# Kernel tuning notes

Measured on AMD Instinct MI355X. Metric: run time of the kernel, lower is better.

Reference implementation:

```python
import jax, jax.numpy as jnp
import numpy as np

B, S, E = 4, 2048, 1024


def setup_inputs() -> dict:
    key = jax.random.key(0)
    ks = jax.random.split(key, 7)
    s = 1.0 / np.sqrt(E)  # torch Linear default init scale (uniform bound)
    inp = {
        "input": jax.random.normal(ks[0], (B, S, E), dtype=jnp.float32),
        "masked": 1,
        "W_q": jax.random.uniform(ks[1], (E, E), jnp.float32, -s, s),
        "b_q": jax.random.uniform(ks[2], (E,), jnp.float32, -s, s),
        "W_k": jax.random.uniform(ks[3], (E, E), jnp.float32, -s, s),
        "b_k": jax.random.uniform(ks[4], (E,), jnp.float32, -s, s),
        "W_v": jax.random.uniform(ks[5], (E, E), jnp.float32, -s, s),
        "b_v": jax.random.uniform(ks[6], (E,), jnp.float32, -s, s),
    }
    return inp


def reference(input, masked, W_q, b_q, W_k, b_k, W_v, b_v):
    # torch.nn.Linear: y = x @ W.T + b
    q = jnp.einsum("bse,fe->bsf", input, W_q) + b_q
    k = jnp.einsum("bse,fe->bsf", input, W_k) + b_k
    v = jnp.einsum("bse,fe->bsf", input, W_v) + b_v
    d = q.shape[-1]
    scores = jnp.einsum("bqd,bkd->bqk", q, k) / jnp.sqrt(jnp.float32(d))
    if masked:
        Sq = scores.shape[1]
        causal = jnp.tril(jnp.ones((Sq, Sq), dtype=bool))  # [S,S], broadcast over batch
        scores = jnp.where(causal, scores, -jnp.inf)
    attn = jax.nn.softmax(scores, axis=-1)
    return jnp.einsum("bqk,bkd->bqd", attn, v)
```

## Files before the change

kernel.cpp:

```cpp
#include <hip/hip_runtime.h>

typedef _Float16 f16;
typedef f16 f16x8 __attribute__((ext_vector_type(8)));
typedef f16 f16x4v __attribute__((ext_vector_type(4)));
typedef float f32x4 __attribute__((ext_vector_type(4)));

__device__ __forceinline__ void async_ld16(const void* g, void* l) {
    __builtin_amdgcn_global_load_lds(
        (const __attribute__((address_space(1))) unsigned int*)g,
        (__attribute__((address_space(3))) unsigned int*)l, 16, 0, 0);
}


#define STG(b, op, kh, P, P1, tOff) do {                                        \
    char* d_ = (char*)smem + (b) * 65536 + (op) * 32768 + (kh) * 16384 + stgBase; \
    async_ld16((P)  + (tOff) * 64 + (kh) * 32, d_);                             \
    async_ld16((P1) + (tOff) * 64 + (kh) * 32, d_ + 8192);                      \
} while (0)
#define RD_A(b, kk) do {                                                        \
    const char* s_ = (const char*)smem + (b) * 65536 + (kk) * 16384 + aOff;     \
    _Pragma("unroll") for (int m_ = 0; m_ < 8; ++m_)                            \
        af[m_] = *(const f16x8*)(s_ + m_ * 1024);                               \
} while (0)
#define RD_B2(b, kk, n0_) do {                                                  \
    const char* s_ = (const char*)smem + (b) * 65536 + 32768 + (kk) * 16384 + bOff; \
    bf[(n0_)]     = *(const f16x8*)(s_ + ((n0_)) * 1024);                       \
    bf[(n0_) + 1] = *(const f16x8*)(s_ + ((n0_) + 1) * 1024);                   \
} while (0)
#define FENCE_MM(n0_) do {                                                      \
    __builtin_amdgcn_s_barrier();                                               \
    asm volatile("s_waitcnt lgkmcnt(0)" ::: "memory");                          \
    __builtin_amdgcn_sched_barrier(0);                                          \
    __builtin_amdgcn_s_setprio(1);                                              \
    _Pragma("unroll") for (int m_ = 0; m_ < 8; ++m_) {                          \
        acc[m_][(n0_)]     = __builtin_amdgcn_mfma_f32_16x16x32_f16(af[m_], bf[(n0_)],     acc[m_][(n0_)],     0, 0, 0); \
        acc[m_][(n0_) + 1] = __builtin_amdgcn_mfma_f32_16x16x32_f16(af[m_], bf[(n0_) + 1], acc[m_][(n0_) + 1], 0, 0, 0); \
    }                                                                           \
    __builtin_amdgcn_s_setprio(0);                                              \
} while (0)
#define VMC(n) asm volatile("s_waitcnt vmcnt(" #n ")" ::: "memory")
#define BAR __builtin_amdgcn_s_barrier()

#define GEMM256_MAIN_LOOP do {                                                  \
    STG(0, 0, 0, pA, pA1, 0); STG(0, 1, 0, pB, pB1, 0);                         \
    STG(0, 0, 1, pA, pA1, 0); STG(0, 1, 1, pB, pB1, 0);                         \
    STG(1, 0, 0, pA, pA1, 1); STG(1, 1, 0, pB, pB1, 1);                         \
    VMC(4);                                                                     \
    BAR;                                                                        \
    _Pragma("unroll 1")                                                         \
    for (int i_ = 0; i_ < 7; ++i_) {                                            \
        RD_A(0, 0); RD_B2(0, 0, 0); STG(1, 0, 1, pA, pA1, 1);           \
        FENCE_MM(0); BAR;                                                       \
        RD_B2(0, 0, 2);             STG(1, 1, 1, pB, pB1, 1);           \
        FENCE_MM(2); BAR;                                                       \
        RD_A(0, 1); RD_B2(0, 1, 0); STG(0, 0, 0, pA, pA1, 2);           \
        FENCE_MM(0); BAR;                                                       \
        RD_B2(0, 1, 2);             STG(0, 1, 0, pB, pB1, 2);           \
        FENCE_MM(2); VMC(4); BAR;                                               \
        RD_A(1, 0); RD_B2(1, 0, 0); STG(0, 0, 1, pA, pA1, 2);           \
        FENCE_MM(0); BAR;                                                       \
        RD_B2(1, 0, 2);             STG(0, 1, 1, pB, pB1, 2);           \
        FENCE_MM(2); BAR;                                                       \
        RD_A(1, 1); RD_B2(1, 1, 0); STG(1, 0, 0, pA, pA1, 3);           \
        FENCE_MM(0); BAR;                                                       \
        RD_B2(1, 1, 2);             STG(1, 1, 0, pB, pB1, 3);           \
        FENCE_MM(2); VMC(4); BAR;                                               \
        pA += 128; pA1 += 128; pB += 128; pB1 += 128;                           \
    }                                                                           \
    RD_A(0, 0); RD_B2(0, 0, 0); STG(1, 0, 1, pA, pA1, 1);                       \
    FENCE_MM(0); BAR;                                                           \
    RD_B2(0, 0, 2);             STG(1, 1, 1, pB, pB1, 1);                       \
    FENCE_MM(2); BAR;                                                           \
    RD_A(0, 1); RD_B2(0, 1, 0);                                                 \
    FENCE_MM(0); BAR;                                                           \
    RD_B2(0, 1, 2);                                                             \
    FENCE_MM(2); VMC(0); BAR;                                                   \
    RD_A(1, 0); RD_B2(1, 0, 0);                                                 \
    FENCE_MM(0); BAR;                                                           \
    RD_B2(1, 0, 2);                                                             \
    FENCE_MM(2); BAR;                                                           \
    RD_A(1, 1); RD_B2(1, 1, 0);                                                 \
    FENCE_MM(0); BAR;                                                           \
    RD_B2(1, 1, 2);                                                             \
    FENCE_MM(2); BAR;        \
} while (0)

#define GEMM256_SETUP                                                           \
    __shared__ __align__(16) f16 smem[65536];                      \
    const int tid = threadIdx.x;                                                \
    const int wave = tid >> 6, lane = tid & 63;                                 \
    const int wrow = wave >> 2, wcol = wave & 3;                                \
    const int quad = lane >> 4, l16 = lane & 15;                                \
    const int rowLane = tid >> 2;                                               \
    const int cOff = ((tid & 3) ^ ((tid >> 3) & 3)) * 8;                        \
    const int stgBase = wave * 1024;                                            \
    const int swz  = (quad ^ ((l16 >> 1) & 3)) * 16;                            \
    const int aOff = (wrow * 128 + l16) * 64 + swz;                             \
    const int bOff = (wcol * 64 + l16) * 64 + swz;                              \
    f32x4 acc[8][4];                                                            \
    _Pragma("unroll") for (int m_i = 0; m_i < 8; ++m_i)                         \
        _Pragma("unroll") for (int n_i = 0; n_i < 4; ++n_i)                     \
            acc[m_i][n_i] = (f32x4){0.f, 0.f, 0.f, 0.f};                        \
    f16x8 af[8], bf[4];

__global__ __launch_bounds__(512, 2) void qkv256(
    const f16* __restrict__ A, const f16* __restrict__ Bt,
    const float* __restrict__ b_q, const float* __restrict__ b_k,
    const float* __restrict__ b_v,
    f16* __restrict__ Q16, f16* __restrict__ K16, f16* __restrict__ Vt16)
{
    int bid = blockIdx.x;
    bid = (bid & 7) * 48 + (bid >> 3);
    const int by = bid / 12, bx = bid - by * 12;
    const int mBase = by * 256, nBase = bx * 256;

    GEMM256_SETUP

    const f16* pA  = A  + (long)(mBase + rowLane) * 1024 + cOff;
    const f16* pA1 = pA + 128 * 1024;
    const f16* pB  = Bt + (long)(nBase + rowLane) * 1024 + cOff;
    const f16* pB1 = pB + 128 * 1024;

    GEMM256_MAIN_LOOP;

    const int seg = nBase >> 10;
    const float* bs = (seg == 0) ? b_q : (seg == 1) ? b_k : b_v;
    const int lcb = (nBase & 1023) + wcol * 64;
    float bvv[4];
#pragma unroll
    for (int n = 0; n < 4; ++n) bvv[n] = bs[lcb + n * 16 + l16];

    if (seg < 2) {
        f16* dst = (seg == 0) ? Q16 : K16;
#pragma unroll
        for (int m = 0; m < 8; ++m)
#pragma unroll
            for (int n = 0; n < 4; ++n)
#pragma unroll
                for (int r = 0; r < 4; ++r) {
                    const int row = mBase + wrow * 128 + m * 16 + quad * 4 + r;
                    dst[(long)row * 1024 + lcb + n * 16 + l16] =
                        (f16)(acc[m][n][r] + bvv[n]);
                }
    } else {
        const int b = mBase >> 11, s0 = mBase & 2047;
        const int e0 = (nBase & 1023) + wcol * 64;
        f16* epiW = smem + wave * (64 * 80);
#pragma unroll
        for (int sb = 0; sb < 2; ++sb) {
#pragma unroll
            for (int m4 = 0; m4 < 4; ++m4)
#pragma unroll
                for (int n = 0; n < 4; ++n) {
                    f16x4v pk;
#pragma unroll
                    for (int r = 0; r < 4; ++r)
                        pk[r] = (f16)(acc[sb * 4 + m4][n][r] + bvv[n]);
                    *(f16x4v*)&epiW[(n * 16 + l16) * 80 + m4 * 16 + quad * 4] = pk;
                }
            asm volatile("s_waitcnt lgkmcnt(0)" ::: "memory");
#pragma unroll
            for (int it = 0; it < 8; ++it) {
                const int e = it * 8 + (lane >> 3);
                const f16x8 v = *(const f16x8*)&epiW[e * 80 + (lane & 7) * 8];
                *(f16x8*)(Vt16 + ((long)b * 1024 + e0 + e) * 2048 + s0 +
                          wrow * 128 + sb * 64 + (lane & 7) * 8) = v;
            }
        }
    }
}

__global__ __launch_bounds__(512, 2) void scores256(
    const f16* __restrict__ Q, const f16* __restrict__ K,
    f16* __restrict__ P, float* __restrict__ rowsum,
    const int* __restrict__ maskedp)
{
    const int masked = *maskedp;
    const int bx = blockIdx.x, by = blockIdx.y, bz = blockIdx.z;
    if (masked && bx > by) return;
    const int mBase = by * 256, nBase = bx * 256;

    GEMM256_SETUP

    const f16* Ab  = Q + (long)bz * (2048L * 1024);
    const f16* Btb = K + (long)bz * (2048L * 1024);
    const f16* pA  = Ab  + (long)(mBase + rowLane) * 1024 + cOff;
    const f16* pA1 = pA + 128 * 1024;
    const f16* pB  = Btb + (long)(nBase + rowLane) * 1024 + cOff;
    const f16* pB1 = pB + 128 * 1024;

    GEMM256_MAIN_LOOP;

    f16* Crow = P + (long)bz * (2048L * 2048);
    float* rsb = rowsum + bz * 2048;
#pragma unroll
    for (int m = 0; m < 8; ++m) {
        float rs[4] = {0.f, 0.f, 0.f, 0.f};
#pragma unroll
        for (int n = 0; n < 4; ++n)
#pragma unroll
            for (int r = 0; r < 4; ++r) {
                const int row = mBase + wrow * 128 + m * 16 + quad * 4 + r;
                const int col = nBase + wcol * 64 + n * 16 + l16;
                float e = __expf(acc[m][n][r] * 0.03125f);
                if (masked && col > row) e = 0.f;
                const f16 hv = (f16)e;
                Crow[(long)row * 2048 + col] = hv;
                rs[r] += (float)hv;
            }
#pragma unroll
        for (int r = 0; r < 4; ++r) {
            float s = rs[r];
            s += __shfl_xor(s, 1);
            s += __shfl_xor(s, 2);
            s += __shfl_xor(s, 4);
            s += __shfl_xor(s, 8);
            if (l16 == 0) {
                const int row = mBase + wrow * 128 + m * 16 + quad * 4 + r;
                atomicAdd(&rsb[row], s);
            }
        }
    }
}

#undef STG
#undef RD_A
#undef RD_B2
#undef FENCE_MM
#undef GEMM256_MAIN_LOOP
#undef GEMM256_SETUP

#define PSTG_A(b, kh, tOff) do {                                                \
    char* d_ = (char*)smem + (b) * 32768 + (kh) * 8192 + stgBase;               \
    async_ld16(pA  + (tOff) * 64 + (kh) * 32, d_);                              \
    async_ld16(pA1 + (tOff) * 64 + (kh) * 32, d_ + 4096);                       \
} while (0)
#define PSTG_B(b, kh, tOff) do {                                                \
    char* d_ = (char*)smem + (b) * 32768 + 16384 + (kh) * 8192 + stgBase;       \
    async_ld16(pB  + (tOff) * 64 + (kh) * 32, d_);                              \
    async_ld16(pB1 + (tOff) * 64 + (kh) * 32, d_ + 4096);                       \
} while (0)
#define PRD(b, kk) do {                                                         \
    const char* sa_ = (const char*)smem + (b) * 32768 + (kk) * 8192 + aOff;     \
    _Pragma("unroll") for (int m_ = 0; m_ < 4; ++m_)                            \
        af[m_] = *(const f16x8*)(sa_ + m_ * 1024);                              \
    const char* sb_ = (const char*)smem + (b) * 32768 + 16384 + (kk) * 8192 + bOff; \
    _Pragma("unroll") for (int n_ = 0; n_ < 4; ++n_)                            \
        bf[n_] = *(const f16x8*)(sb_ + n_ * 1024);                              \
} while (0)
#define PFENCE do {                                                             \
    __builtin_amdgcn_s_barrier();                                               \
    asm volatile("s_waitcnt lgkmcnt(0)" ::: "memory");                          \
    __builtin_amdgcn_sched_barrier(0);                                          \
    __builtin_amdgcn_s_setprio(1);                                              \
    _Pragma("unroll") for (int m_ = 0; m_ < 4; ++m_)                            \
        _Pragma("unroll") for (int n_ = 0; n_ < 4; ++n_)                        \
            acc[m_][n_] = __builtin_amdgcn_mfma_f32_16x16x32_f16(af[m_], bf[n_], acc[m_][n_], 0, 0, 0); \
    __builtin_amdgcn_s_setprio(0);                                              \
} while (0)

__global__ __launch_bounds__(256, 2) void pv128(
    const f16* __restrict__ P, const f16* __restrict__ Vt,
    const float* __restrict__ rowsum, float* __restrict__ out,
    const int* __restrict__ maskedp)
{
    const int masked = *maskedp;
    const int bx = blockIdx.x, bz = blockIdx.z;
    const int by = gridDim.y - 1 - blockIdx.y;
    const int mBase = by * 128, nBase = bx * 128;
    const int nIter = masked ? ((by >> 1) + 1) * 2 : 16;

    __shared__ __align__(16) f16 smem[32768];
    const int tid = threadIdx.x;
    const int wave = tid >> 6, lane = tid & 63;
    const int wrow = wave >> 1, wcol = wave & 1;
    const int quad = lane >> 4, l16 = lane & 15;
    const int rowLane = tid >> 2;
    const int cOff = ((tid & 3) ^ ((tid >> 3) & 3)) * 8;
    const int stgBase = wave * 1024;
    const int swz  = (quad ^ ((l16 >> 1) & 3)) * 16;
    const int aOff = (wrow * 64 + l16) * 64 + swz;
    const int bOff = (wcol * 64 + l16) * 64 + swz;

    const f16* Pb = P  + (long)bz * (2048L * 2048);
    const f16* Vb = Vt + (long)bz * (1024L * 2048);
    const f16* pA  = Pb + (long)(mBase + rowLane) * 2048 + cOff;
    const f16* pA1 = pA + 64 * 2048;
    const f16* pB  = Vb + (long)(nBase + rowLane) * 2048 + cOff;
    const f16* pB1 = pB + 64 * 2048;

    f32x4 acc[4][4];
#pragma unroll
    for (int m = 0; m < 4; ++m)
#pragma unroll
        for (int n = 0; n < 4; ++n) acc[m][n] = (f32x4){0.f, 0.f, 0.f, 0.f};
    f16x8 af[4], bf[4];

    PSTG_A(0, 0, 0); PSTG_B(0, 0, 0);
    PSTG_A(0, 1, 0); PSTG_B(0, 1, 0);
    PSTG_A(1, 0, 1); PSTG_B(1, 0, 1);
    VMC(4);
    BAR;

#pragma unroll 1
    for (int i = 0; i < nIter - 1; ++i) {
        PRD(0, 0); PSTG_A(1, 1, 1); PSTG_B(1, 1, 1);
        PFENCE; VMC(8); BAR;
        PRD(0, 1); PSTG_A(0, 0, 2); PSTG_B(0, 0, 2);
        PFENCE; VMC(8); BAR;
        PRD(1, 0); PSTG_A(0, 1, 2); PSTG_B(0, 1, 2);
        PFENCE; VMC(8); BAR;
        PRD(1, 1); PSTG_A(1, 0, 3); PSTG_B(1, 0, 3);
        PFENCE; VMC(8); BAR;
        pA += 128; pA1 += 128; pB += 128; pB1 += 128;
    }
    PRD(0, 0); PSTG_A(1, 1, 1); PSTG_B(1, 1, 1);
    PFENCE; VMC(8); BAR;
    PRD(0, 1);
    PFENCE; VMC(4); BAR;
    PRD(1, 0);
    PFENCE; VMC(0); BAR;
    PRD(1, 1);
    PFENCE;

    const float* rsb = rowsum + bz * 2048;
    float* ob = out + (long)bz * (2048L * 1024);
#pragma unroll
    for (int m = 0; m < 4; ++m)
#pragma unroll
        for (int r = 0; r < 4; ++r) {
            const int row = mBase + wrow * 64 + m * 16 + quad * 4 + r;
            const float inv = 1.f / rsb[row];
#pragma unroll
            for (int n = 0; n < 4; ++n) {
                const int col = nBase + wcol * 64 + n * 16 + l16;
                ob[(long)row * 1024 + col] = acc[m][n][r] * inv;
            }
        }
}

#undef PSTG_A
#undef PSTG_B
#undef PRD
#undef PFENCE
#undef VMC
#undef BAR

__global__ void cvt_inp(const float* __restrict__ in, f16* __restrict__ out, int n4)
{
    const int i = blockIdx.x * blockDim.x + threadIdx.x;
    if (i >= n4) return;
    const float4 v = ((const float4*)in)[i];
    f16x4v o;
    o[0] = (f16)v.x; o[1] = (f16)v.y; o[2] = (f16)v.z; o[3] = (f16)v.w;
    ((f16x4v*)out)[i] = o;
}

__global__ void cvt_w3(const float* __restrict__ W0, const float* __restrict__ W1,
                       const float* __restrict__ W2, f16* __restrict__ out)
{
    const int bxx = blockIdx.x;
    const int which = bxx >> 10;
    const float* src = (which == 0) ? W0 : (which == 1) ? W1 : W2;
    const int i = (bxx & 1023) * 256 + threadIdx.x;
    const float4 v = ((const float4*)src)[i];
    f16x4v o;
    o[0] = (f16)v.x; o[1] = (f16)v.y; o[2] = (f16)v.z; o[3] = (f16)v.w;
    ((f16x4v*)(out + (long)which * 1024 * 1024))[i] = o;
}

extern "C" void kernel_launch(void* const* d_in, const int* in_sizes, int n_in,
                              void* d_out, int out_size, void* d_ws, size_t ws_size,
                              hipStream_t stream)
{
    const float* inp = (const float*)d_in[0];
    const int* masked = (const int*)d_in[1];
    const float* Wq = (const float*)d_in[2];
    const float* bq = (const float*)d_in[3];
    const float* Wk = (const float*)d_in[4];
    const float* bk = (const float*)d_in[5];
    const float* Wv = (const float*)d_in[6];
    const float* bv = (const float*)d_in[7];
    float* out = (float*)d_out;

    const int Bb = 4, S = 2048, E = 1024;
    const long nTok = (long)Bb * S;

    char* ws = (char*)d_ws;
    f16* inp16 = (f16*)ws;   ws += nTok * E * 2;
    f16* W3    = (f16*)ws;   ws += (long)3 * E * E * 2;
    f16* Q16   = (f16*)ws;   ws += nTok * E * 2;
    f16* K16   = (f16*)ws;   ws += nTok * E * 2;
    f16* Vt16  = (f16*)ws;   ws += nTok * E * 2;
    f16* P16   = (f16*)ws;   ws += (long)Bb * S * S * 2;
    float* rsum = (float*)ws; ws += nTok * 4;

    dim3 blk(256);

    hipMemsetAsync(rsum, 0, nTok * 4, stream);
    cvt_inp<<<(int)(nTok * E / 4 / 256), blk, 0, stream>>>(inp, inp16, (int)(nTok * E / 4));
    cvt_w3<<<3 * 1024, blk, 0, stream>>>(Wq, Wk, Wv, W3);

    qkv256<<<dim3(32 * 12), dim3(512), 0, stream>>>(
        inp16, W3, bq, bk, bv, Q16, K16, Vt16);

    scores256<<<dim3(8, 8, 4), dim3(512), 0, stream>>>(
        Q16, K16, P16, rsum, masked);

    pv128<<<dim3(8, 16, 4), dim3(256), 0, stream>>>(
        P16, Vt16, rsum, out, masked);
}
```

Before: 241.5 us.

## Replace 256x256 QKV GEMM tile with 128x256 tile kernel

The fused QKV projection GEMM moves from a 256x256 block tile to a 128x256 tile, doubling the grid from 384 to 768 blocks. This gives better wave coverage of the CUs, where 384 blocks would leave a partial second wave. The new kernel has a smaller LDS footprint, a 4x4 MFMA accumulator per wave, and a simpler four-phase pipeline with adjusted vmcnt waits. The smaller tile has lower arithmetic intensity, so operand traffic per FLOP goes up. The shared macros are inlined into the scores kernel.

```diff
diff --git a/kernel.cpp b/kernel.cpp
--- a/kernel.cpp
+++ b/kernel.cpp
@@ -11,6 +11,8 @@
         (__attribute__((address_space(3))) unsigned int*)l, 16, 0, 0);
 }
 
+#define VMC(n) asm volatile("s_waitcnt vmcnt(" #n ")" ::: "memory")
+#define BAR __builtin_amdgcn_s_barrier()
 
 #define STG(b, op, kh, P, P1, tOff) do {                                        \
     char* d_ = (char*)smem + (b) * 65536 + (op) * 32768 + (kh) * 16384 + stgBase; \
@@ -38,137 +40,6 @@
     }                                                                           \
     __builtin_amdgcn_s_setprio(0);                                              \
 } while (0)
-#define VMC(n) asm volatile("s_waitcnt vmcnt(" #n ")" ::: "memory")
-#define BAR __builtin_amdgcn_s_barrier()
-
-#define GEMM256_MAIN_LOOP do {                                                  \
-    STG(0, 0, 0, pA, pA1, 0); STG(0, 1, 0, pB, pB1, 0);                         \
-    STG(0, 0, 1, pA, pA1, 0); STG(0, 1, 1, pB, pB1, 0);                         \
-    STG(1, 0, 0, pA, pA1, 1); STG(1, 1, 0, pB, pB1, 1);                         \
-    VMC(4);                                                                     \
-    BAR;                                                                        \
-    _Pragma("unroll 1")                                                         \
-    for (int i_ = 0; i_ < 7; ++i_) {                                            \
-        RD_A(0, 0); RD_B2(0, 0, 0); STG(1, 0, 1, pA, pA1, 1);           \
-        FENCE_MM(0); BAR;                                                       \
-        RD_B2(0, 0, 2);             STG(1, 1, 1, pB, pB1, 1);           \
-        FENCE_MM(2); BAR;                                                       \
-        RD_A(0, 1); RD_B2(0, 1, 0); STG(0, 0, 0, pA, pA1, 2);           \
-        FENCE_MM(0); BAR;                                                       \
-        RD_B2(0, 1, 2);             STG(0, 1, 0, pB, pB1, 2);           \
-        FENCE_MM(2); VMC(4); BAR;                                               \
-        RD_A(1, 0); RD_B2(1, 0, 0); STG(0, 0, 1, pA, pA1, 2);           \
-        FENCE_MM(0); BAR;                                                       \
-        RD_B2(1, 0, 2);             STG(0, 1, 1, pB, pB1, 2);           \
-        FENCE_MM(2); BAR;                                                       \
-        RD_A(1, 1); RD_B2(1, 1, 0); STG(1, 0, 0, pA, pA1, 3);           \
-        FENCE_MM(0); BAR;                                                       \
-        RD_B2(1, 1, 2);             STG(1, 1, 0, pB, pB1, 3);           \
-        FENCE_MM(2); VMC(4); BAR;                                               \
-        pA += 128; pA1 += 128; pB += 128; pB1 += 128;                           \
-    }                                                                           \
-    RD_A(0, 0); RD_B2(0, 0, 0); STG(1, 0, 1, pA, pA1, 1);                       \
-    FENCE_MM(0); BAR;                                                           \
-    RD_B2(0, 0, 2);             STG(1, 1, 1, pB, pB1, 1);                       \
-    FENCE_MM(2); BAR;                                                           \
-    RD_A(0, 1); RD_B2(0, 1, 0);                                                 \
-    FENCE_MM(0); BAR;                                                           \
-    RD_B2(0, 1, 2);                                                             \
-    FENCE_MM(2); VMC(0); BAR;                                                   \
-    RD_A(1, 0); RD_B2(1, 0, 0);                                                 \
-    FENCE_MM(0); BAR;                                                           \
-    RD_B2(1, 0, 2);                                                             \
-    FENCE_MM(2); BAR;                                                           \
-    RD_A(1, 1); RD_B2(1, 1, 0);                                                 \
-    FENCE_MM(0); BAR;                                                           \
-    RD_B2(1, 1, 2);                                                             \
-    FENCE_MM(2); BAR;        \
-} while (0)
-
-#define GEMM256_SETUP                                                           \
-    __shared__ __align__(16) f16 smem[65536];                      \
-    const int tid = threadIdx.x;                                                \
-    const int wave = tid >> 6, lane = tid & 63;                                 \
-    const int wrow = wave >> 2, wcol = wave & 3;                                \
-    const int quad = lane >> 4, l16 = lane & 15;                                \
-    const int rowLane = tid >> 2;                                               \
-    const int cOff = ((tid & 3) ^ ((tid >> 3) & 3)) * 8;                        \
-    const int stgBase = wave * 1024;                                            \
-    const int swz  = (quad ^ ((l16 >> 1) & 3)) * 16;                            \
-    const int aOff = (wrow * 128 + l16) * 64 + swz;                             \
-    const int bOff = (wcol * 64 + l16) * 64 + swz;                              \
-    f32x4 acc[8][4];                                                            \
-    _Pragma("unroll") for (int m_i = 0; m_i < 8; ++m_i)                         \
-        _Pragma("unroll") for (int n_i = 0; n_i < 4; ++n_i)                     \
-            acc[m_i][n_i] = (f32x4){0.f, 0.f, 0.f, 0.f};                        \
-    f16x8 af[8], bf[4];
-
-__global__ __launch_bounds__(512, 2) void qkv256(
-    const f16* __restrict__ A, const f16* __restrict__ Bt,
-    const float* __restrict__ b_q, const float* __restrict__ b_k,
-    const float* __restrict__ b_v,
-    f16* __restrict__ Q16, f16* __restrict__ K16, f16* __restrict__ Vt16)
-{
-    int bid = blockIdx.x;
-    bid = (bid & 7) * 48 + (bid >> 3);
-    const int by = bid / 12, bx = bid - by * 12;
-    const int mBase = by * 256, nBase = bx * 256;
-
-    GEMM256_SETUP
-
-    const f16* pA  = A  + (long)(mBase + rowLane) * 1024 + cOff;
-    const f16* pA1 = pA + 128 * 1024;
-    const f16* pB  = Bt + (long)(nBase + rowLane) * 1024 + cOff;
-    const f16* pB1 = pB + 128 * 1024;
-
-    GEMM256_MAIN_LOOP;
-
-    const int seg = nBase >> 10;
-    const float* bs = (seg == 0) ? b_q : (seg == 1) ? b_k : b_v;
-    const int lcb = (nBase & 1023) + wcol * 64;
-    float bvv[4];
-#pragma unroll
-    for (int n = 0; n < 4; ++n) bvv[n] = bs[lcb + n * 16 + l16];
-
-    if (seg < 2) {
-        f16* dst = (seg == 0) ? Q16 : K16;
-#pragma unroll
-        for (int m = 0; m < 8; ++m)
-#pragma unroll
-            for (int n = 0; n < 4; ++n)
-#pragma unroll
-                for (int r = 0; r < 4; ++r) {
-                    const int row = mBase + wrow * 128 + m * 16 + quad * 4 + r;
-                    dst[(long)row * 1024 + lcb + n * 16 + l16] =
-                        (f16)(acc[m][n][r] + bvv[n]);
-                }
-    } else {
-        const int b = mBase >> 11, s0 = mBase & 2047;
-        const int e0 = (nBase & 1023) + wcol * 64;
-        f16* epiW = smem + wave * (64 * 80);
-#pragma unroll
-        for (int sb = 0; sb < 2; ++sb) {
-#pragma unroll
-            for (int m4 = 0; m4 < 4; ++m4)
-#pragma unroll
-                for (int n = 0; n < 4; ++n) {
-                    f16x4v pk;
-#pragma unroll
-                    for (int r = 0; r < 4; ++r)
-                        pk[r] = (f16)(acc[sb * 4 + m4][n][r] + bvv[n]);
-                    *(f16x4v*)&epiW[(n * 16 + l16) * 80 + m4 * 16 + quad * 4] = pk;
-                }
-            asm volatile("s_waitcnt lgkmcnt(0)" ::: "memory");
-#pragma unroll
-            for (int it = 0; it < 8; ++it) {
-                const int e = it * 8 + (lane >> 3);
-                const f16x8 v = *(const f16x8*)&epiW[e * 80 + (lane & 7) * 8];
-                *(f16x8*)(Vt16 + ((long)b * 1024 + e0 + e) * 2048 + s0 +
-                          wrow * 128 + sb * 64 + (lane & 7) * 8) = v;
-            }
-        }
-    }
-}
 
 __global__ __launch_bounds__(512, 2) void scores256(
     const f16* __restrict__ Q, const f16* __restrict__ K,
@@ -180,7 +51,23 @@
     if (masked && bx > by) return;
     const int mBase = by * 256, nBase = bx * 256;
 
-    GEMM256_SETUP
+    __shared__ __align__(16) f16 smem[65536];
+    const int tid = threadIdx.x;
+    const int wave = tid >> 6, lane = tid & 63;
+    const int wrow = wave >> 2, wcol = wave & 3;
+    const int quad = lane >> 4, l16 = lane & 15;
+    const int rowLane = tid >> 2;
+    const int cOff = ((tid & 3) ^ ((tid >> 3) & 3)) * 8;
+    const int stgBase = wave * 1024;
+    const int swz  = (quad ^ ((l16 >> 1) & 3)) * 16;
+    const int aOff = (wrow * 128 + l16) * 64 + swz;
+    const int bOff = (wcol * 64 + l16) * 64 + swz;
+    f32x4 acc[8][4];
+#pragma unroll
+    for (int m = 0; m < 8; ++m)
+#pragma unroll
+        for (int n = 0; n < 4; ++n) acc[m][n] = (f32x4){0.f, 0.f, 0.f, 0.f};
+    f16x8 af[8], bf[4];
 
     const f16* Ab  = Q + (long)bz * (2048L * 1024);
     const f16* Btb = K + (long)bz * (2048L * 1024);
@@ -189,7 +76,48 @@
     const f16* pB  = Btb + (long)(nBase + rowLane) * 1024 + cOff;
     const f16* pB1 = pB + 128 * 1024;
 
-    GEMM256_MAIN_LOOP;
+    STG(0, 0, 0, pA, pA1, 0); STG(0, 1, 0, pB, pB1, 0);
+    STG(0, 0, 1, pA, pA1, 0); STG(0, 1, 1, pB, pB1, 0);
+    STG(1, 0, 0, pA, pA1, 1); STG(1, 1, 0, pB, pB1, 1);
+    VMC(4);
+    BAR;
+
+#pragma unroll 1
+    for (int i = 0; i < 7; ++i) {
+        RD_A(0, 0); RD_B2(0, 0, 0); STG(1, 0, 1, pA, pA1, 1);
+        FENCE_MM(0); BAR;
+        RD_B2(0, 0, 2);             STG(1, 1, 1, pB, pB1, 1);
+        FENCE_MM(2); BAR;
+        RD_A(0, 1); RD_B2(0, 1, 0); STG(0, 0, 0, pA, pA1, 2);
+        FENCE_MM(0); BAR;
+        RD_B2(0, 1, 2);             STG(0, 1, 0, pB, pB1, 2);
+        FENCE_MM(2); VMC(4); BAR;
+        RD_A(1, 0); RD_B2(1, 0, 0); STG(0, 0, 1, pA, pA1, 2);
+        FENCE_MM(0); BAR;
+        RD_B2(1, 0, 2);             STG(0, 1, 1, pB, pB1, 2);
+        FENCE_MM(2); BAR;
+        RD_A(1, 1); RD_B2(1, 1, 0); STG(1, 0, 0, pA, pA1, 3);
+        FENCE_MM(0); BAR;
+        RD_B2(1, 1, 2);             STG(1, 1, 0, pB, pB1, 3);
+        FENCE_MM(2); VMC(4); BAR;
+        pA += 128; pA1 += 128; pB += 128; pB1 += 128;
+    }
+    RD_A(0, 0); RD_B2(0, 0, 0); STG(1, 0, 1, pA, pA1, 1);
+    FENCE_MM(0); BAR;
+    RD_B2(0, 0, 2);             STG(1, 1, 1, pB, pB1, 1);
+    FENCE_MM(2); BAR;
+    RD_A(0, 1); RD_B2(0, 1, 0);
+    FENCE_MM(0); BAR;
+    RD_B2(0, 1, 2);
+    FENCE_MM(2); VMC(0); BAR;
+    RD_A(1, 0); RD_B2(1, 0, 0);
+    FENCE_MM(0); BAR;
+    RD_B2(1, 0, 2);
+    FENCE_MM(2); BAR;
+    RD_A(1, 1); RD_B2(1, 1, 0);
+    FENCE_MM(0); BAR;
+    RD_B2(1, 1, 2);
+    FENCE_MM(2);
 
     f16* Crow = P + (long)bz * (2048L * 2048);
     float* rsb = rowsum + bz * 2048;
@@ -227,8 +155,146 @@
 #undef RD_A
 #undef RD_B2
 #undef FENCE_MM
-#undef GEMM256_MAIN_LOOP
-#undef GEMM256_SETUP
+
+#define QSTG_A(b, kh, tOff) do {                                                \
+    char* d_ = (char*)smem + (b) * 49152 + (kh) * 8192 + stgBase;               \
+    async_ld16(pA + (tOff) * 64 + (kh) * 32, d_);                               \
+} while (0)
+#define QSTG_B(b, kh, tOff) do {                                                \
+    char* d_ = (char*)smem + (b) * 49152 + 16384 + (kh) * 16384 + stgBase;      \
+    async_ld16(pB  + (tOff) * 64 + (kh) * 32, d_);                              \
+    async_ld16(pB1 + (tOff) * 64 + (kh) * 32, d_ + 8192);                       \
+} while (0)
+#define QRD(b, kk) do {                                                         \
+    const char* sa_ = (const char*)smem + (b) * 49152 + (kk) * 8192 + aOff;     \
+    _Pragma("unroll") for (int m_ = 0; m_ < 4; ++m_)                            \
+        af[m_] = *(const f16x8*)(sa_ + m_ * 1024);                              \
+    const char* sb_ = (const char*)smem + (b) * 49152 + 16384 + (kk) * 16384 + bOff; \
+    _Pragma("unroll") for (int n_ = 0; n_ < 4; ++n_)                            \
+        bf[n_] = *(const f16x8*)(sb_ + n_ * 1024);                              \
+} while (0)
+#define QFENCE do {                                                             \
+    __builtin_amdgcn_s_barrier();                                               \
+    asm volatile("s_waitcnt lgkmcnt(0)" ::: "memory");                          \
+    __builtin_amdgcn_sched_barrier(0);                                          \
+    __builtin_amdgcn_s_setprio(1);                                              \
+    _Pragma("unroll") for (int m_ = 0; m_ < 4; ++m_)                            \
+        _Pragma("unroll") for (int n_ = 0; n_ < 4; ++n_)                        \
+            acc[m_][n_] = __builtin_amdgcn_mfma_f32_16x16x32_f16(af[m_], bf[n_], acc[m_][n_], 0, 0, 0); \
+    __builtin_amdgcn_s_setprio(0);                                              \
+} while (0)
+
+__global__ __launch_bounds__(512, 2) void qkv128(
+    const f16* __restrict__ A, const f16* __restrict__ Bt,
+    const float* __restrict__ b_q, const float* __restrict__ b_k,
+    const float* __restrict__ b_v,
+    f16* __restrict__ Q16, f16* __restrict__ K16, f16* __restrict__ Vt16)
+{
+    int bid = blockIdx.x;
+    bid = (bid & 7) * 96 + (bid >> 3);
+    const int by = bid / 12, bx = bid - by * 12;
+    const int mBase = by * 128, nBase = bx * 256;
+
+    __shared__ __align__(16) f16 smem[49152];
+    const int tid = threadIdx.x;
+    const int wave = tid >> 6, lane = tid & 63;
+    const int wrow = wave >> 2, wcol = wave & 3;
+    const int quad = lane >> 4, l16 = lane & 15;
+    const int rowLane = tid >> 2;
+    const int cOff = ((tid & 3) ^ ((tid >> 3) & 3)) * 8;
+    const int stgBase = wave * 1024;
+    const int swz  = (quad ^ ((l16 >> 1) & 3)) * 16;
+    const int aOff = (wrow * 64 + l16) * 64 + swz;
+    const int bOff = (wcol * 64 + l16) * 64 + swz;
+
+    const f16* pA  = A  + (long)(mBase + rowLane) * 1024 + cOff;
+    const f16* pB  = Bt + (long)(nBase + rowLane) * 1024 + cOff;
+    const f16* pB1 = pB + 128 * 1024;
+
+    f32x4 acc[4][4];
+#pragma unroll
+    for (int m = 0; m < 4; ++m)
+#pragma unroll
+        for (int n = 0; n < 4; ++n) acc[m][n] = (f32x4){0.f, 0.f, 0.f, 0.f};
+    f16x8 af[4], bf[4];
+
+    QSTG_A(0, 0, 0); QSTG_B(0, 0, 0);
+    QSTG_A(0, 1, 0); QSTG_B(0, 1, 0);
+    QSTG_A(1, 0, 1); QSTG_B(1, 0, 1);
+    VMC(3);
+    BAR;
+
+#pragma unroll 1
+    for (int i = 0; i < 7; ++i) {
+        QRD(0, 0); QSTG_A(1, 1, 1); QSTG_B(1, 1, 1);
+        QFENCE; VMC(6); BAR;
+        QRD(0, 1); QSTG_A(0, 0, 2); QSTG_B(0, 0, 2);
+        QFENCE; VMC(6); BAR;
+        QRD(1, 0); QSTG_A(0, 1, 2); QSTG_B(0, 1, 2);
+        QFENCE; VMC(6); BAR;
+        QRD(1, 1); QSTG_A(1, 0, 3); QSTG_B(1, 0, 3);
+        QFENCE; VMC(6); BAR;
+        pA += 128; pB += 128; pB1 += 128;
+    }
+    QRD(0, 0); QSTG_A(1, 1, 1); QSTG_B(1, 1, 1);
+    QFENCE; VMC(6); BAR;
+    QRD(0, 1);
+    QFENCE; VMC(3); BAR;
+    QRD(1, 0);
+    QFENCE; VMC(0); BAR;
+    QRD(1, 1);
+    QFENCE;
+    BAR;
+
+    const int seg = nBase >> 10;
+    const float* bs = (seg == 0) ? b_q : (seg == 1) ? b_k : b_v;
+    const int lcb = (nBase & 1023) + wcol * 64;
+    float bvv[4];
+#pragma unroll
+    for (int n = 0; n < 4; ++n) bvv[n] = bs[lcb + n * 16 + l16];
+
+    if (seg < 2) {
+        f16* dst = (seg == 0) ? Q16 : K16;
+#pragma unroll
+        for (int m = 0; m < 4; ++m)
+#pragma unroll
+            for (int n = 0; n < 4; ++n)
+#pragma unroll
+                for (int r = 0; r < 4; ++r) {
+                    const int row = mBase + wrow * 64 + m * 16 + quad * 4 + r;
+                    dst[(long)row * 1024 + lcb + n * 16 + l16] =
+                        (f16)(acc[m][n][r] + bvv[n]);
+                }
+    } else {
+        const int b = mBase >> 11;
+        const int s0 = (mBase & 2047) + wrow * 64;
+        const int e0 = (nBase & 1023) + wcol * 64;
+        f16* epiW = smem + wave * (64 * 72);
+#pragma unroll
+        for (int m = 0; m < 4; ++m)
+#pragma unroll
+            for (int n = 0; n < 4; ++n) {
+                f16x4v pk;
+#pragma unroll
+                for (int r = 0; r < 4; ++r)
+                    pk[r] = (f16)(acc[m][n][r] + bvv[n]);
+                *(f16x4v*)&epiW[(n * 16 + l16) * 72 + m * 16 + quad * 4] = pk;
+            }
+        asm volatile("s_waitcnt lgkmcnt(0)" ::: "memory");
+#pragma unroll
+        for (int it = 0; it < 8; ++it) {
+            const int e = it * 8 + (lane >> 3);
+            const f16x8 v = *(const f16x8*)&epiW[e * 72 + (lane & 7) * 8];
+            *(f16x8*)(Vt16 + ((long)b * 1024 + e0 + e) * 2048 + s0 +
+                      (lane & 7) * 8) = v;
+        }
+    }
+}
+
+#undef QSTG_A
+#undef QSTG_B
+#undef QRD
+#undef QFENCE
 
 #define PSTG_A(b, kh, tOff) do {                                                \
     char* d_ = (char*)smem + (b) * 32768 + (kh) * 8192 + stgBase;               \
@@ -401,7 +467,7 @@
     cvt_inp<<<(int)(nTok * E / 4 / 256), blk, 0, stream>>>(inp, inp16, (int)(nTok * E / 4));
     cvt_w3<<<3 * 1024, blk, 0, stream>>>(Wq, Wk, Wv, W3);
 
-    qkv256<<<dim3(32 * 12), dim3(512), 0, stream>>>(
+    qkv128<<<dim3(768), dim3(512), 0, stream>>>(
         inp16, W3, bq, bk, bv, Q16, K16, Vt16);
 
     scores256<<<dim3(8, 8, 4), dim3(512), 0, stream>>>(
```

New measurement: 252.8 us. 1.05x slower.
